# Performance work log

Measured on AMD Instinct MI355X. Metric: run time of the kernel, lower is better.

## Reference

```python
import jax, jax.numpy as jnp
import numpy as np

E, TOPK, R = 8, 2, 16          # num_experts, top_k, rank_per_expert
D, H, GH = 1024, 16, 256       # embed_dim, num_heads, gating hidden
HD = D // H
SCALE = HD ** -0.5


def setup_inputs() -> dict:
    key = jax.random.key(0)
    ks = jax.random.split(key, 32)
    B, S = 32, 257
    inp = {"hidden_states": jax.random.normal(ks[0], (B, S, D), jnp.float32)}
    # gating network params
    inp["gw1"] = jax.random.normal(ks[1], (GH, D), jnp.float32) * 0.02
    inp["gb1"] = jnp.zeros((GH,), jnp.float32)
    inp["gw2"] = jax.random.normal(ks[2], (E, GH), jnp.float32) * 0.02
    inp["gb2"] = jnp.zeros((E,), jnp.float32)
    # four SVDMoeLinear projections: main weight, expert U/S/V, bias
    i = 3
    for p in ("q", "k", "v", "o"):
        inp[p + "Wm"] = jax.random.normal(ks[i], (D, D), jnp.float32) * 0.02; i += 1
        inp[p + "U"] = jax.random.normal(ks[i], (E, D, R), jnp.float32) * 0.02; i += 1
        inp[p + "S"] = jax.random.normal(ks[i], (E, R), jnp.float32) * 0.1; i += 1
        inp[p + "V"] = jax.random.normal(ks[i], (E, R, D), jnp.float32) * 0.02; i += 1
        inp[p + "b"] = jnp.zeros((D,), jnp.float32)
    return inp


def _svd_moe(x, Wm, U, S, V, b, idx, gates):
    # x: (B,S,D); idx,gates: (B,k); U:(E,D,R) S:(E,R) V:(E,R,D)
    main = jnp.einsum('bsd,od->bso', x, Wm)
    Ug, Sg, Vg = U[idx], S[idx], V[idx]        # (B,k,D,R), (B,k,R), (B,k,R,D)
    xv = jnp.einsum('bsd,bkrd->bksr', x, Vg)   # project into expert subspace
    xvs = xv * Sg[:, :, None, :]
    eo = jnp.einsum('bksr,bkor->bkso', xvs, Ug)
    expert = jnp.einsum('bkso,bk->bso', eo, gates)
    return main + expert + b


def reference(hidden_states, gw1, gb1, gw2, gb2,
              qWm, qU, qS, qV, qb,
              kWm, kU, kS, kV, kb,
              vWm, vU, vS, vV, vb,
              oWm, oU, oS, oV, ob):
    B, S, _ = hidden_states.shape
    # per-sample gating on pooled features
    pooled = hidden_states.mean(axis=1)
    h = jax.nn.relu(pooled @ gw1.T + gb1)
    logits = h @ gw2.T + gb2                    # (B,E)
    top_vals, top_idx = jax.lax.top_k(logits, TOPK)
    gates = jax.nn.softmax(top_vals, axis=-1)   # (B,k)

    q = _svd_moe(hidden_states, qWm, qU, qS, qV, qb, top_idx, gates) * SCALE
    k = _svd_moe(hidden_states, kWm, kU, kS, kV, kb, top_idx, gates)
    v = _svd_moe(hidden_states, vWm, vU, vS, vV, vb, top_idx, gates)

    def shp(t):
        return t.reshape(B, S, H, HD).transpose(0, 2, 1, 3)  # (B,H,S,HD)
    q, k, v = shp(q), shp(k), shp(v)
    attn = jax.nn.softmax(jnp.einsum('bhsd,bhtd->bhst', q, k), axis=-1)
    ctx = jnp.einsum('bhst,bhtd->bhsd', attn, v)
    ctx = ctx.transpose(0, 2, 1, 3).reshape(B, S, D)
    out = _svd_moe(ctx, oWm, oU, oS, oV, ob, top_idx, gates)
    return out
```

## Files before the change

kernel.cpp:

```cpp
#include <hip/hip_runtime.h>
#include <math.h>

#define Bb   32
#define SQ   257
#define SQV  320
#define Dm   1024
#define HD   64
#define Ee   8
#define Rr   16
#define GHh  256
#define NT   (Bb*SQ)
#define KX   1152
#define LDP  72

typedef unsigned short ush;
typedef _Float16 h16;
typedef __attribute__((ext_vector_type(8))) _Float16 half8;
typedef __attribute__((ext_vector_type(4))) _Float16 half4;
typedef __attribute__((ext_vector_type(8))) short short8;
typedef __attribute__((ext_vector_type(4))) float floatx4;
typedef __attribute__((ext_vector_type(16))) float floatx16;

__device__ __forceinline__ ush f2h(float f) {
    union { h16 h; ush u; } a; a.h = (h16)f; return a.u;
}
__device__ __forceinline__ void store_h4(ush* p, float4 v) {
    half4 h; h.x = (h16)v.x; h.y = (h16)v.y; h.z = (h16)v.z; h.w = (h16)v.w;
    *(half4*)p = h;
}
__device__ __forceinline__ void load16(const ush* g, ush* l) {
    __builtin_amdgcn_global_load_lds(
        (const __attribute__((address_space(1))) unsigned int*)g,
        (__attribute__((address_space(3))) unsigned int*)l,
        16, 0, 0);
}

__global__ __launch_bounds__(256) void zero_kernel(ush* __restrict__ p)
{
    const size_t i = ((size_t)blockIdx.x * 256 + threadIdx.x) * 8;
    short8 z = {0,0,0,0,0,0,0,0};
    *(short8*)(p + i) = z;
}

__global__ __launch_bounds__(256) void pool_kernel(
    const float* __restrict__ x, float* __restrict__ pp, ush* __restrict__ xf)
{
    const int c = blockIdx.x, b = blockIdx.y, t = threadIdx.x;
    const int s0 = c * 16, s1 = (c == 15) ? SQ : s0 + 16;
    float4 acc = make_float4(0.f, 0.f, 0.f, 0.f);
    const float* xp = x + ((size_t)b * SQ + s0) * Dm + t * 4;
    ush* xo = xf + ((size_t)b * SQ + s0) * Dm + t * 4;
    for (int s = s0; s < s1; ++s, xp += Dm, xo += Dm) {
        float4 v = *(const float4*)xp;
        store_h4(xo, v);
        acc.x += v.x; acc.y += v.y; acc.z += v.z; acc.w += v.w;
    }
    *(float4*)(pp + ((size_t)b * 16 + c) * Dm + t * 4) = acc;
}

__global__ __launch_bounds__(256) void gating2_kernel(
    const float* __restrict__ pp, const float* __restrict__ gw1,
    const float* __restrict__ gb1, const float* __restrict__ gw2,
    const float* __restrict__ gb2,
    float* __restrict__ gates, int* __restrict__ idx)
{
    __shared__ float pooled[Dm];
    __shared__ float hbuf[GHh];
    __shared__ float logits[Ee];
    const int b = blockIdx.x, t = threadIdx.x;
    const int w = t >> 6, lane = t & 63;

    float4 acc = make_float4(0.f, 0.f, 0.f, 0.f);
    for (int c = 0; c < 16; ++c) {
        float4 v = *(const float4*)(pp + ((size_t)b * 16 + c) * Dm + t * 4);
        acc.x += v.x; acc.y += v.y; acc.z += v.z; acc.w += v.w;
    }
    const float sc = 1.0f / SQ;
    pooled[t*4+0] = acc.x * sc; pooled[t*4+1] = acc.y * sc;
    pooled[t*4+2] = acc.z * sc; pooled[t*4+3] = acc.w * sc;
    __syncthreads();

    for (int oi = 0; oi < 64; ++oi) {
        const int o = w * 64 + oi;
        const float* g = gw1 + (size_t)o * Dm;
        float s = 0.f;
        #pragma unroll
        for (int i = 0; i < 16; ++i) s += pooled[lane + i*64] * g[lane + i*64];
        for (int off = 32; off > 0; off >>= 1) s += __shfl_down(s, off, 64);
        if (lane == 0) hbuf[o] = fmaxf(s + gb1[o], 0.f);
    }
    __syncthreads();
    if (t < Ee) {
        const float* g = gw2 + t * GHh;
        float s = 0.f;
        for (int j = 0; j < GHh; ++j) s += hbuf[j] * g[j];
        logits[t] = s + gb2[t];
    }
    __syncthreads();
    if (t == 0) {
        int i1 = 0; float v1 = logits[0];
        for (int e = 1; e < Ee; ++e) if (logits[e] > v1) { v1 = logits[e]; i1 = e; }
        int i2 = 0; float v2 = -1e30f;
        for (int e = 0; e < Ee; ++e) if (e != i1 && logits[e] > v2) { v2 = logits[e]; i2 = e; }
        float e2 = __expf(v2 - v1);
        float inv = 1.f / (1.f + e2);
        gates[b*2+0] = inv; gates[b*2+1] = e2 * inv;
        idx[b*2+0] = i1; idx[b*2+1] = i2;
    }
}

__global__ __launch_bounds__(256) void convBV_kernel(
    const float* __restrict__ W0, const float* __restrict__ U0,
    const float* __restrict__ W1, const float* __restrict__ U1,
    const float* __restrict__ W2, const float* __restrict__ U2,
    const float* __restrict__ W3, const float* __restrict__ U3,
    const float* __restrict__ V0, const float* __restrict__ V1,
    const float* __restrict__ V2, const float* __restrict__ V3,
    ush* __restrict__ Bf0, ush* __restrict__ Bf1,
    ush* __restrict__ Bf2, ush* __restrict__ Bf3,
    ush* __restrict__ Vf)
{
    const int p = blockIdx.y;
    if (blockIdx.x < 1152) {
        const float* W = p == 0 ? W0 : p == 1 ? W1 : p == 2 ? W2 : W3;
        const float* U = p == 0 ? U0 : p == 1 ? U1 : p == 2 ? U2 : U3;
        ush* Bf = p == 0 ? Bf0 : p == 1 ? Bf1 : p == 2 ? Bf2 : Bf3;
        const int i = blockIdx.x * 256 + threadIdx.x;
        const int n = i / 288, c4 = i % 288, col = c4 * 4;
        float4 v;
        if (col < Dm) {
            v = *(const float4*)(W + (size_t)n * Dm + col);
        } else {
            int ec = col - Dm, e = ec >> 4, r = ec & 15;
            v = *(const float4*)(U + ((size_t)(e * Dm + n)) * Rr + r);
        }
        store_h4(Bf + (size_t)n * KX + col, v);
    } else {
        const float* V = p == 0 ? V0 : p == 1 ? V1 : p == 2 ? V2 : V3;
        const size_t i = ((size_t)(blockIdx.x - 1152) * 256 + threadIdx.x) * 4;
        float4 v = *(const float4*)(V + i);
        store_h4(Vf + (size_t)p * Ee * Rr * Dm + i, v);
    }
}

template<int NP>
__global__ __launch_bounds__(256) void ext_gemm(
    const ush* __restrict__ xf,
    const ush* __restrict__ Vf,
    const float* __restrict__ S0, const float* __restrict__ S1,
    const float* __restrict__ S2,
    ush* __restrict__ o0, ush* __restrict__ o1, ush* __restrict__ o2,
    const float* __restrict__ gates, const int* __restrict__ idx, int pbase)
{
    __shared__ ush sA[2*64*32], sB[2*NP*16*32];
    const int mt = blockIdx.x, b = blockIdx.y, kk = blockIdx.z;
    const int t = threadIdx.x, lane = t & 63, w = t >> 6;
    const int quad = lane >> 4, l16 = lane & 15;
    const int s0 = mt * 64;
    const int e = idx[b*2+kk];
    const float g = gates[b*2+kk];

    const int rl = lane >> 2;
    const int swsrc = ((lane & 3) ^ ((lane >> 3) & 3)) * 8;
    const int swrd  = ((quad ^ ((l16 >> 1) & 3)) * 8);

    int sa = s0 + w * 16 + rl; if (sa > SQ - 1) sa = SQ - 1;
    const ush* aptr = xf + ((size_t)(b * SQ + sa)) * Dm + swsrc;
    const ush* bptr = (w < NP)
        ? Vf + ((size_t)(pbase + w)) * Ee * Rr * Dm + ((size_t)(e * Rr + rl)) * Dm + swsrc
        : nullptr;
    ush* la0 = &sA[w * 512];
    ush* la1 = &sA[2048 + w * 512];
    ush* lb0 = (w < NP) ? &sB[w * 512] : nullptr;
    ush* lb1 = (w < NP) ? &sB[NP*512 + w * 512] : nullptr;

    floatx4 S[NP] = {};

    for (int it = 0; it < 16; ++it) {
        __syncthreads();
        load16(aptr, la0); load16(aptr + 32, la1); aptr += 64;
        if (w < NP) {
            load16(bptr, lb0); load16(bptr + 32, lb1); bptr += 64;
        }
        __syncthreads();
        #pragma unroll
        for (int j = 0; j < 2; ++j) {
            const half8 a = *(const half8*)&sA[j*2048 + (w*16 + l16)*32 + swrd];
            #pragma unroll
            for (int p = 0; p < NP; ++p) {
                const half8 bb = *(const half8*)&sB[j*NP*512 + (p*16 + l16)*32 + swrd];
                S[p] = __builtin_amdgcn_mfma_f32_16x16x32_f16(a, bb, S[p], 0, 0, 0);
            }
        }
    }

    #pragma unroll
    for (int p = 0; p < NP; ++p) {
        const float* Sp = p == 0 ? S0 : p == 1 ? S1 : S2;
        const float scale = g * Sp[e * Rr + l16];
        ush* oo = p == 0 ? o0 : p == 1 ? o1 : o2;
        #pragma unroll
        for (int r = 0; r < 4; ++r) {
            const int s = s0 + w * 16 + quad * 4 + r;
            if (s < SQ)
                oo[((size_t)(b * SQ + s)) * 128 + e * 16 + l16] = f2h(S[p][r] * scale);
        }
    }
}

template<int MODE>
__global__ __launch_bounds__(256) void gemm_mfma(
    const ush* __restrict__ A,
    const ush* __restrict__ E0, const ush* __restrict__ E1, const ush* __restrict__ E2,
    const ush* __restrict__ B0, const ush* __restrict__ B1, const ush* __restrict__ B2,
    const float* __restrict__ b0, const float* __restrict__ b1, const float* __restrict__ b2,
    ush* __restrict__ y0, ush* __restrict__ y1, ush* __restrict__ vt,
    float* __restrict__ yo, float qscale)
{
    const int stripe = blockIdx.x % 72;
    if (stripe >= 65) return;
    const int nb = blockIdx.x / 72;
    const int z = blockIdx.z;
    const ush* E = z == 0 ? E0 : z == 1 ? E1 : E2;
    const ush* Bm = z == 0 ? B0 : z == 1 ? B1 : B2;
    const float* bias = z == 0 ? b0 : z == 1 ? b1 : b2;

    __shared__ ush sLDS[2*128*64];
    ush* sA = sLDS;
    ush* sB = sLDS + 128*64;
    const int t = threadIdx.x, lane = t & 63, w = t >> 6;
    const int m0 = stripe * 128, n0 = nb * 128;
    const int row8 = lane >> 3, c8l = lane & 7;
    const int swk = (c8l ^ row8) * 8;
    const int wm = w >> 1, wn = w & 1;
    const int l31 = lane & 31, h5 = lane >> 5;

    const ush* ap[4]; const ush* ep[4]; const ush* bp[4];
    ush *la[4], *lb[4];
    #pragma unroll
    for (int c = 0; c < 4; ++c) {
        const int j = c * 4 + w;
        const int rowl = j * 8 + row8;
        int rga = m0 + rowl; if (rga > NT - 1) rga = NT - 1;
        ap[c] = A + (size_t)rga * Dm + swk;
        ep[c] = E + (size_t)rga * 128 + swk;
        bp[c] = Bm + (size_t)(n0 + rowl) * KX + swk;
        la[c] = &sA[j * 512];
        lb[c] = &sB[j * 512];
    }

    int aofs[4][2], bofs[4][2];
    #pragma unroll
    for (int s = 0; s < 4; ++s)
        #pragma unroll
        for (int i = 0; i < 2; ++i) {
            const int g = s * 2 + h5;
            aofs[s][i] = (wm*64 + i*32 + l31) * 64 + ((g ^ (l31 & 7)) * 8);
            bofs[s][i] = (wn*64 + i*32 + l31) * 64 + ((g ^ (l31 & 7)) * 8);
        }

    floatx16 acc[2][2] = {};

    for (int it = 0; it < 16; ++it) {
        __syncthreads();
        #pragma unroll
        for (int c = 0; c < 4; ++c) {
            load16(ap[c], la[c]); ap[c] += 64;
            load16(bp[c], lb[c]); bp[c] += 64;
        }
        __syncthreads();
        #pragma unroll
        for (int s = 0; s < 4; ++s) {
            half8 af0 = *(const half8*)&sA[aofs[s][0]];
            half8 af1 = *(const half8*)&sA[aofs[s][1]];
            half8 bf0 = *(const half8*)&sB[bofs[s][0]];
            half8 bf1 = *(const half8*)&sB[bofs[s][1]];
            acc[0][0] = __builtin_amdgcn_mfma_f32_32x32x16_f16(af0, bf0, acc[0][0], 0, 0, 0);
            acc[0][1] = __builtin_amdgcn_mfma_f32_32x32x16_f16(af0, bf1, acc[0][1], 0, 0, 0);
            acc[1][0] = __builtin_amdgcn_mfma_f32_32x32x16_f16(af1, bf0, acc[1][0], 0, 0, 0);
            acc[1][1] = __builtin_amdgcn_mfma_f32_32x32x16_f16(af1, bf1, acc[1][1], 0, 0, 0);
        }
    }
    for (int it = 0; it < 2; ++it) {
        __syncthreads();
        #pragma unroll
        for (int c = 0; c < 4; ++c) {
            load16(ep[c], la[c]); ep[c] += 64;
            load16(bp[c], lb[c]); bp[c] += 64;
        }
        __syncthreads();
        #pragma unroll
        for (int s = 0; s < 4; ++s) {
            half8 af0 = *(const half8*)&sA[aofs[s][0]];
            half8 af1 = *(const half8*)&sA[aofs[s][1]];
            half8 bf0 = *(const half8*)&sB[bofs[s][0]];
            half8 bf1 = *(const half8*)&sB[bofs[s][1]];
            acc[0][0] = __builtin_amdgcn_mfma_f32_32x32x16_f16(af0, bf0, acc[0][0], 0, 0, 0);
            acc[0][1] = __builtin_amdgcn_mfma_f32_32x32x16_f16(af0, bf1, acc[0][1], 0, 0, 0);
            acc[1][0] = __builtin_amdgcn_mfma_f32_32x32x16_f16(af1, bf0, acc[1][0], 0, 0, 0);
            acc[1][1] = __builtin_amdgcn_mfma_f32_32x32x16_f16(af1, bf1, acc[1][1], 0, 0, 0);
        }
    }

    if (MODE == 1) {
        #pragma unroll
        for (int mi = 0; mi < 2; ++mi) {
            #pragma unroll
            for (int ni = 0; ni < 2; ++ni) {
                const int col = n0 + wn*64 + ni*32 + l31;
                const float bsv = bias[col];
                const int rb = m0 + wm*64 + mi*32 + 4*h5;
                #pragma unroll
                for (int r = 0; r < 16; ++r) {
                    const int row = rb + (r & 3) + 8 * (r >> 2);
                    if (row < NT)
                        yo[(size_t)row * Dm + col] = acc[mi][ni][r] + bsv;
                }
            }
        }
    } else {
        __syncthreads();
        #pragma unroll
        for (int mi = 0; mi < 2; ++mi) {
            #pragma unroll
            for (int ni = 0; ni < 2; ++ni) {
                const int colL = wn*64 + ni*32 + l31;
                const float bsv = bias[n0 + colL];
                const int rbL = wm*64 + mi*32 + 4*h5;
                #pragma unroll
                for (int r = 0; r < 16; ++r) {
                    const int rowL = rbL + (r & 3) + 8 * (r >> 2);
                    float val = acc[mi][ni][r] + bsv;
                    if (z == 0) val *= qscale;
                    sLDS[rowL*128 + ((((colL>>3) ^ (rowL&7)) << 3) | (colL & 7))] = f2h(val);
                }
            }
        }
        __syncthreads();
        if (z != 2) {
            ush* y = (z == 0) ? y0 : y1;
            #pragma unroll
            for (int i = 0; i < 8; ++i) {
                const int u = i*256 + t;
                const int rowL = u >> 4, cj = u & 15;
                const int row = m0 + rowL;
                if (row < NT) {
                    half8 v = *(const half8*)&sLDS[rowL*128 + ((cj ^ (rowL&7)) << 3)];
                    *(half8*)(y + (size_t)row * Dm + n0 + cj*8) = v;
                }
            }
        } else {
            #pragma unroll
            for (int i = 0; i < 8; ++i) {
                const int u = i*256 + t;
                const int oct = u & 15, colL = u >> 4;
                const int colg = n0 + colL;
                const int h_ = colg >> 6, d_ = colg & 63;
                const size_t vrow = (size_t)h_ * 64 + d_;
                #pragma unroll
                for (int jj = 0; jj < 8; ++jj) {
                    const int rowL = oct + jj*16;
                    const int row = m0 + rowL;
                    if (row < NT) {
                        const int b_ = row / SQ, s_ = row - b_*SQ;
                        vt[((size_t)b_*1024 + vrow) * SQV + s_] =
                            sLDS[rowL*128 + ((((colL>>3) ^ (rowL&7)) << 3) | (colL & 7))];
                    }
                }
            }
        }
    }
}

__global__ __launch_bounds__(256) void attn_mfma(
    const ush* __restrict__ q, const ush* __restrict__ k,
    const ush* __restrict__ vt, ush* __restrict__ cf)
{
    __shared__ ush sK[64*LDP], sVt[64*LDP];
    __shared__ ush sP[4][16*LDP];
    const int qt = blockIdx.x, h = blockIdx.y, b = blockIdx.z;
    const int t = threadIdx.x, lane = t & 63, w = t >> 6;
    const int quad = lane >> 4, l16 = lane & 15;
    const size_t base = (size_t)b * SQ * Dm + (size_t)h * HD;
    const size_t vbase = ((size_t)(b * 16 + h)) * 64 * SQV;

    #pragma unroll
    for (int i = 0; i < 2; ++i) {
        const int u = t + i * 256;
        const int row = u >> 3, c8 = u & 7;
        int s = qt * 64 + row; if (s > SQ - 1) s = SQ - 1;
        short8 ld = *(const short8*)(q + base + (size_t)s * Dm + c8 * 8);
        *(short8*)&sK[row*LDP + c8*8] = ld;
    }
    __syncthreads();
    half8 qf[2];
    #pragma unroll
    for (int s = 0; s < 2; ++s)
        qf[s] = *(const half8*)&sK[(w*16 + l16)*LDP + s*32 + quad*8];

    floatx4 O[4] = {};
    float mrow[4], lrow[4];
    #pragma unroll
    for (int r = 0; r < 4; ++r) { mrow[r] = -1e30f; lrow[r] = 0.f; }
    const bool active = (qt * 64 + w * 16) < SQ;

    for (int kt = 0; kt < 5; ++kt) {
        __syncthreads();
        #pragma unroll
        for (int i = 0; i < 2; ++i) {
            const int u = t + i * 256;
            const int row = u >> 3, c8 = u & 7;
            const int s = kt * 64 + row;
            short8 kv = {0,0,0,0,0,0,0,0};
            if (s < SQ) kv = *(const short8*)(k + base + (size_t)s * Dm + c8 * 8);
            *(short8*)&sK[row*LDP + c8*8] = kv;
            short8 vv = *(const short8*)(vt + vbase + (size_t)row * SQV + kt*64 + c8*8);
            *(short8*)&sVt[row*LDP + c8*8] = vv;
        }
        __syncthreads();
        if (!active) continue;

        floatx4 S[4] = {};
        #pragma unroll
        for (int ni = 0; ni < 4; ++ni)
            #pragma unroll
            for (int s = 0; s < 2; ++s) {
                half8 kf = *(const half8*)&sK[(ni*16 + l16)*LDP + s*32 + quad*8];
                S[ni] = __builtin_amdgcn_mfma_f32_16x16x32_f16(qf[s], kf, S[ni], 0, 0, 0);
            }
        #pragma unroll
        for (int ni = 0; ni < 4; ++ni) {
            const int jg = kt * 64 + ni * 16 + l16;
            if (jg >= SQ) { S[ni][0] = -1e30f; S[ni][1] = -1e30f; S[ni][2] = -1e30f; S[ni][3] = -1e30f; }
        }
        float mnew[4], alpha[4];
        #pragma unroll
        for (int r = 0; r < 4; ++r) {
            float mx = fmaxf(fmaxf(S[0][r], S[1][r]), fmaxf(S[2][r], S[3][r]));
            #pragma unroll
            for (int off = 1; off < 16; off <<= 1) mx = fmaxf(mx, __shfl_xor(mx, off, 64));
            mnew[r] = fmaxf(mrow[r], mx);
            alpha[r] = __expf(mrow[r] - mnew[r]);
            mrow[r] = mnew[r];
        }
        float p[4][4], rs[4];
        #pragma unroll
        for (int r = 0; r < 4; ++r) rs[r] = 0.f;
        #pragma unroll
        for (int ni = 0; ni < 4; ++ni)
            #pragma unroll
            for (int r = 0; r < 4; ++r) {
                float e = __expf(S[ni][r] - mnew[r]);
                p[ni][r] = e; rs[r] += e;
            }
        #pragma unroll
        for (int r = 0; r < 4; ++r) {
            #pragma unroll
            for (int off = 1; off < 16; off <<= 1) rs[r] += __shfl_xor(rs[r], off, 64);
            lrow[r] = lrow[r] * alpha[r] + rs[r];
        }
        #pragma unroll
        for (int ni = 0; ni < 4; ++ni)
            #pragma unroll
            for (int r = 0; r < 4; ++r) O[ni][r] *= alpha[r];
        #pragma unroll
        for (int ni = 0; ni < 4; ++ni)
            #pragma unroll
            for (int r = 0; r < 4; ++r)
                sP[w][(quad*4 + r)*LDP + ni*16 + l16] = f2h(p[ni][r]);
        #pragma unroll
        for (int ni = 0; ni < 4; ++ni)
            #pragma unroll
            for (int s = 0; s < 2; ++s) {
                half8 a  = *(const half8*)&sP[w][l16*LDP + s*32 + quad*8];
                half8 bb = *(const half8*)&sVt[(ni*16 + l16)*LDP + s*32 + quad*8];
                O[ni] = __builtin_amdgcn_mfma_f32_16x16x32_f16(a, bb, O[ni], 0, 0, 0);
            }
    }

    if (active) {
        #pragma unroll
        for (int ni = 0; ni < 4; ++ni) {
            const int col = h * HD + ni * 16 + l16;
            #pragma unroll
            for (int r = 0; r < 4; ++r) {
                const int s = qt * 64 + w * 16 + quad * 4 + r;
                if (s < SQ)
                    cf[((size_t)(b * SQ + s)) * Dm + col] = f2h(O[ni][r] / lrow[r]);
            }
        }
    }
}

extern "C" void kernel_launch(void* const* d_in, const int* in_sizes, int n_in,
                              void* d_out, int out_size, void* d_ws, size_t ws_size,
                              hipStream_t stream)
{
    const float* x   = (const float*)d_in[0];
    const float* gw1 = (const float*)d_in[1];
    const float* gb1 = (const float*)d_in[2];
    const float* gw2 = (const float*)d_in[3];
    const float* gb2 = (const float*)d_in[4];
    const float *Wm[4], *U[4], *Sv[4], *Vv[4], *bias[4];
    for (int p = 0; p < 4; ++p) {
        Wm[p]   = (const float*)d_in[5 + p*5 + 0];
        U[p]    = (const float*)d_in[5 + p*5 + 1];
        Sv[p]   = (const float*)d_in[5 + p*5 + 2];
        Vv[p]   = (const float*)d_in[5 + p*5 + 3];
        bias[p] = (const float*)d_in[5 + p*5 + 4];
    }
    char* wsb   = (char*)d_ws;
    float* gates = (float*)wsb;
    int*   idx   = (int*)(wsb + 256);
    float* pool  = (float*)(wsb + 1024);
    ush* p = (ush*)(wsb + 1024 + (size_t)Bb * 16 * Dm * 4);
    ush* xf = p; p += (size_t)NT * Dm;
    ush* ef[4];
    for (int i = 0; i < 4; ++i) { ef[i] = p; p += (size_t)NT * 128; }
    ush* Bf[4];
    for (int i = 0; i < 4; ++i) { Bf[i] = p; p += (size_t)1024 * KX; }
    ush* Vf = p; p += (size_t)4 * Ee * Rr * Dm;
    ush* qf = p; p += (size_t)NT * Dm;
    ush* kf = p; p += (size_t)NT * Dm;
    ush* vt = p; p += (size_t)Bb * 16 * 64 * SQV;

    zero_kernel<<<2056, 256, 0, stream>>>(ef[0]);
    pool_kernel<<<dim3(16, Bb), 256, 0, stream>>>(x, pool, xf);
    gating2_kernel<<<Bb, 256, 0, stream>>>(pool, gw1, gb1, gw2, gb2, gates, idx);
    convBV_kernel<<<dim3(1280, 4), 256, 0, stream>>>(
        Wm[0], U[0], Wm[1], U[1], Wm[2], U[2], Wm[3], U[3],
        Vv[0], Vv[1], Vv[2], Vv[3],
        Bf[0], Bf[1], Bf[2], Bf[3], Vf);

    ext_gemm<3><<<dim3(5, Bb, 2), 256, 0, stream>>>(xf, Vf,
        Sv[0], Sv[1], Sv[2], ef[0], ef[1], ef[2], gates, idx, 0);

    gemm_mfma<0><<<dim3(576, 1, 3), 256, 0, stream>>>(
        xf, ef[0], ef[1], ef[2], Bf[0], Bf[1], Bf[2],
        bias[0], bias[1], bias[2], qf, kf, vt, nullptr, 0.125f);

    attn_mfma<<<dim3(5, 16, Bb), 256, 0, stream>>>(qf, kf, vt, xf);

    ext_gemm<1><<<dim3(5, Bb, 2), 256, 0, stream>>>(xf, Vf,
        Sv[3], Sv[3], Sv[3], ef[3], ef[3], ef[3], gates, idx, 3);

    gemm_mfma<1><<<dim3(576, 1, 1), 256, 0, stream>>>(
        xf, ef[3], ef[3], ef[3], Bf[3], Bf[3], Bf[3],
        bias[3], bias[3], bias[3], nullptr, nullptr, nullptr, (float*)d_out, 1.0f);
}
```

Baseline: 387.8 us.

## Fuse prep kernels, zero unused expert slots in ext_gemm, prefetch K/V in attention

```diff
diff --git a/kernel.cpp b/kernel.cpp
--- a/kernel.cpp
+++ b/kernel.cpp
@@ -35,27 +35,55 @@
         16, 0, 0);
 }
 
-__global__ __launch_bounds__(256) void zero_kernel(ush* __restrict__ p)
+__global__ __launch_bounds__(256) void prep_kernel(
+    const float* __restrict__ x, float* __restrict__ pp, ush* __restrict__ xf,
+    const float* __restrict__ W0, const float* __restrict__ U0,
+    const float* __restrict__ W1, const float* __restrict__ U1,
+    const float* __restrict__ W2, const float* __restrict__ U2,
+    const float* __restrict__ W3, const float* __restrict__ U3,
+    const float* __restrict__ V0, const float* __restrict__ V1,
+    const float* __restrict__ V2, const float* __restrict__ V3,
+    ush* __restrict__ Bf0, ush* __restrict__ Bf1,
+    ush* __restrict__ Bf2, ush* __restrict__ Bf3,
+    ush* __restrict__ Vf)
 {
-    const size_t i = ((size_t)blockIdx.x * 256 + threadIdx.x) * 8;
-    short8 z = {0,0,0,0,0,0,0,0};
-    *(short8*)(p + i) = z;
-}
-
-__global__ __launch_bounds__(256) void pool_kernel(
-    const float* __restrict__ x, float* __restrict__ pp, ush* __restrict__ xf)
-{
-    const int c = blockIdx.x, b = blockIdx.y, t = threadIdx.x;
-    const int s0 = c * 16, s1 = (c == 15) ? SQ : s0 + 16;
-    float4 acc = make_float4(0.f, 0.f, 0.f, 0.f);
-    const float* xp = x + ((size_t)b * SQ + s0) * Dm + t * 4;
-    ush* xo = xf + ((size_t)b * SQ + s0) * Dm + t * 4;
-    for (int s = s0; s < s1; ++s, xp += Dm, xo += Dm) {
-        float4 v = *(const float4*)xp;
-        store_h4(xo, v);
-        acc.x += v.x; acc.y += v.y; acc.z += v.z; acc.w += v.w;
-    }
-    *(float4*)(pp + ((size_t)b * 16 + c) * Dm + t * 4) = acc;
+    const int bid = blockIdx.x, t = threadIdx.x;
+    if (bid < 512) {
+        const int c = bid & 15, b = bid >> 4;
+        const int s0 = c * 16, s1 = (c == 15) ? SQ : s0 + 16;
+        float4 acc = make_float4(0.f, 0.f, 0.f, 0.f);
+        const float* xp = x + ((size_t)b * SQ + s0) * Dm + t * 4;
+        ush* xo = xf + ((size_t)b * SQ + s0) * Dm + t * 4;
+        for (int s = s0; s < s1; ++s, xp += Dm, xo += Dm) {
+            float4 v = *(const float4*)xp;
+            store_h4(xo, v);
+            acc.x += v.x; acc.y += v.y; acc.z += v.z; acc.w += v.w;
+        }
+        *(float4*)(pp + ((size_t)b * 16 + c) * Dm + t * 4) = acc;
+        return;
+    }
+    const int bx = bid - 512;
+    const int p = bx / 1280, xb = bx % 1280;
+    if (xb < 1152) {
+        const float* W = p == 0 ? W0 : p == 1 ? W1 : p == 2 ? W2 : W3;
+        const float* U = p == 0 ? U0 : p == 1 ? U1 : p == 2 ? U2 : U3;
+        ush* Bf = p == 0 ? Bf0 : p == 1 ? Bf1 : p == 2 ? Bf2 : Bf3;
+        const int i = xb * 256 + t;
+        const int n = i / 288, c4 = i % 288, col = c4 * 4;
+        float4 v;
+        if (col < Dm) {
+            v = *(const float4*)(W + (size_t)n * Dm + col);
+        } else {
+            int ec = col - Dm, e = ec >> 4, r = ec & 15;
+            v = *(const float4*)(U + ((size_t)(e * Dm + n)) * Rr + r);
+        }
+        store_h4(Bf + (size_t)n * KX + col, v);
+    } else {
+        const float* V = p == 0 ? V0 : p == 1 ? V1 : p == 2 ? V2 : V3;
+        const size_t i = ((size_t)(xb - 1152) * 256 + t) * 4;
+        float4 v = *(const float4*)(V + i);
+        store_h4(Vf + (size_t)p * Ee * Rr * Dm + i, v);
+    }
 }
 
 __global__ __launch_bounds__(256) void gating2_kernel(
@@ -106,40 +134,6 @@
         float inv = 1.f / (1.f + e2);
         gates[b*2+0] = inv; gates[b*2+1] = e2 * inv;
         idx[b*2+0] = i1; idx[b*2+1] = i2;
-    }
-}
-
-__global__ __launch_bounds__(256) void convBV_kernel(
-    const float* __restrict__ W0, const float* __restrict__ U0,
-    const float* __restrict__ W1, const float* __restrict__ U1,
-    const float* __restrict__ W2, const float* __restrict__ U2,
-    const float* __restrict__ W3, const float* __restrict__ U3,
-    const float* __restrict__ V0, const float* __restrict__ V1,
-    const float* __restrict__ V2, const float* __restrict__ V3,
-    ush* __restrict__ Bf0, ush* __restrict__ Bf1,
-    ush* __restrict__ Bf2, ush* __restrict__ Bf3,
-    ush* __restrict__ Vf)
-{
-    const int p = blockIdx.y;
-    if (blockIdx.x < 1152) {
-        const float* W = p == 0 ? W0 : p == 1 ? W1 : p == 2 ? W2 : W3;
-        const float* U = p == 0 ? U0 : p == 1 ? U1 : p == 2 ? U2 : U3;
-        ush* Bf = p == 0 ? Bf0 : p == 1 ? Bf1 : p == 2 ? Bf2 : Bf3;
-        const int i = blockIdx.x * 256 + threadIdx.x;
-        const int n = i / 288, c4 = i % 288, col = c4 * 4;
-        float4 v;
-        if (col < Dm) {
-            v = *(const float4*)(W + (size_t)n * Dm + col);
-        } else {
-            int ec = col - Dm, e = ec >> 4, r = ec & 15;
-            v = *(const float4*)(U + ((size_t)(e * Dm + n)) * Rr + r);
-        }
-        store_h4(Bf + (size_t)n * KX + col, v);
-    } else {
-        const float* V = p == 0 ? V0 : p == 1 ? V1 : p == 2 ? V2 : V3;
-        const size_t i = ((size_t)(blockIdx.x - 1152) * 256 + threadIdx.x) * 4;
-        float4 v = *(const float4*)(V + i);
-        store_h4(Vf + (size_t)p * Ee * Rr * Dm + i, v);
     }
 }
 
@@ -160,6 +154,26 @@
     const int e = idx[b*2+kk];
     const float g = gates[b*2+kk];
 
+    if (kk == 0) {
+        const int e0 = idx[b*2+0], e1 = idx[b*2+1];
+        int zexp[6]; int nz = 0;
+        #pragma unroll
+        for (int ez = 0; ez < Ee; ++ez)
+            if (ez != e0 && ez != e1) zexp[nz++] = ez;
+        short8 zv = {0,0,0,0,0,0,0,0};
+        for (int u = t; u < NP*64*6; u += 256) {
+            const int ei = u % 6; int rest = u / 6;
+            const int r64 = rest & 63; const int p = rest >> 6;
+            const int s = s0 + r64;
+            if (s < SQ) {
+                ush* oo = p == 0 ? o0 : p == 1 ? o1 : o2;
+                ush* dst = oo + ((size_t)(b*SQ + s)) * 128 + zexp[ei]*16;
+                *(short8*)dst = zv;
+                *(short8*)(dst + 8) = zv;
+            }
+        }
+    }
+
     const int rl = lane >> 2;
     const int swsrc = ((lane & 3) ^ ((lane >> 3) & 3)) * 8;
     const int swrd  = ((quad ^ ((l16 >> 1) & 3)) * 8);
@@ -404,8 +418,8 @@
     for (int r = 0; r < 4; ++r) { mrow[r] = -1e30f; lrow[r] = 0.f; }
     const bool active = (qt * 64 + w * 16) < SQ;
 
-    for (int kt = 0; kt < 5; ++kt) {
-        __syncthreads();
+    short8 kreg[2], vreg[2];
+    auto prefetch = [&](int kt) {
         #pragma unroll
         for (int i = 0; i < 2; ++i) {
             const int u = t + i * 256;
@@ -413,10 +427,22 @@
             const int s = kt * 64 + row;
             short8 kv = {0,0,0,0,0,0,0,0};
             if (s < SQ) kv = *(const short8*)(k + base + (size_t)s * Dm + c8 * 8);
-            *(short8*)&sK[row*LDP + c8*8] = kv;
-            short8 vv = *(const short8*)(vt + vbase + (size_t)row * SQV + kt*64 + c8*8);
-            *(short8*)&sVt[row*LDP + c8*8] = vv;
-        }
+            kreg[i] = kv;
+            vreg[i] = *(const short8*)(vt + vbase + (size_t)row * SQV + kt*64 + c8*8);
+        }
+    };
+    prefetch(0);
+
+    for (int kt = 0; kt < 5; ++kt) {
+        __syncthreads();
+        #pragma unroll
+        for (int i = 0; i < 2; ++i) {
+            const int u = t + i * 256;
+            const int row = u >> 3, c8 = u & 7;
+            *(short8*)&sK[row*LDP + c8*8] = kreg[i];
+            *(short8*)&sVt[row*LDP + c8*8] = vreg[i];
+        }
+        if (kt < 4) prefetch(kt + 1);
         __syncthreads();
         if (!active) continue;
 
@@ -524,13 +550,12 @@
     ush* kf = p; p += (size_t)NT * Dm;
     ush* vt = p; p += (size_t)Bb * 16 * 64 * SQV;
 
-    zero_kernel<<<2056, 256, 0, stream>>>(ef[0]);
-    pool_kernel<<<dim3(16, Bb), 256, 0, stream>>>(x, pool, xf);
-    gating2_kernel<<<Bb, 256, 0, stream>>>(pool, gw1, gb1, gw2, gb2, gates, idx);
-    convBV_kernel<<<dim3(1280, 4), 256, 0, stream>>>(
+    prep_kernel<<<5632, 256, 0, stream>>>(
+        x, pool, xf,
         Wm[0], U[0], Wm[1], U[1], Wm[2], U[2], Wm[3], U[3],
         Vv[0], Vv[1], Vv[2], Vv[3],
         Bf[0], Bf[1], Bf[2], Bf[3], Vf);
+    gating2_kernel<<<Bb, 256, 0, stream>>>(pool, gw1, gb1, gw2, gb2, gates, idx);
 
     ext_gemm<3><<<dim3(5, Bb, 2), 256, 0, stream>>>(xf, Vf,
         Sv[0], Sv[1], Sv[2], ef[0], ef[1], ef[2], gates, idx, 0);
```

Result: no change. 384.0 us (-1.0%).
